# Kernel tuning notes

Hardware: AMD Instinct MI355X
Metric: run time of the kernel (lower is better)

The kernel has to match this reference:

```python
import jax, jax.numpy as jnp
import numpy as np

B, T, K, D = 32, 512, 4, 256
E, M = 100000, 2048
NEG = -10000000000.0


def setup_inputs() -> dict:
    key = jax.random.key(0)
    ks = jax.random.split(key, 8)
    token_reprs = jax.random.normal(ks[0], (B, T, K, D), dtype=jnp.float32)
    edge_index = jax.random.randint(ks[1], (2, E), 0, B * T, dtype=jnp.int64)
    lm_indices = jax.random.randint(ks[2], (M,), 0, B * T * K, dtype=jnp.int64)
    batch_pointers = jax.random.randint(ks[3], (M,), 0, B, dtype=jnp.int64)
    tree_padding_mask = jax.random.bernoulli(ks[4], 0.8, (B, T))
    # SwiGLU(2*dim, 4*dim, 1) parameters (no biases)
    sg = 1.0 / np.sqrt(2 * D)
    sh = 1.0 / np.sqrt(4 * D)
    Wg = jax.random.normal(ks[5], (2 * D, 4 * D), dtype=jnp.float32) * sg
    Wv = jax.random.normal(ks[6], (2 * D, 4 * D), dtype=jnp.float32) * sg
    Wo = jax.random.normal(ks[7], (4 * D, 1), dtype=jnp.float32) * sh
    return {
        "token_reprs": token_reprs,
        "Wg": Wg,
        "Wv": Wv,
        "Wo": Wo,
        "edge_index": edge_index,
        "lm_indices": lm_indices,
        "batch_pointers": batch_pointers,
        "tree_padding_mask": tree_padding_mask,
    }


def reference(token_reprs, Wg, Wv, Wo, edge_index, lm_indices, batch_pointers, tree_padding_mask):
    b, t, k, d = token_reprs.shape
    # predict_lemmas: gather type reprs via edge_index, concat, SwiGLU MLP
    type_flat = token_reprs[:, :, 0].reshape(b * t, d)           # [B*T, D]
    scope_ids, goal_ids = edge_index[0], edge_index[1]
    x = jnp.concatenate([type_flat[scope_ids], type_flat[goal_ids]], axis=-1)  # [E, 2D]
    h = jax.nn.silu(x @ Wg) * (x @ Wv)                           # [E, 4D]
    lemmas = (h @ Wo).squeeze(-1)                                # [E]
    # predict_masks: gathers + masked dot-product scoring
    mask_reprs = token_reprs.reshape(-1, d)[lm_indices]          # [M, D]
    type_reprs = token_reprs[:, :, 0]                            # [B, T, D]
    candidates = type_reprs[batch_pointers]                      # [M, T, D]
    candidate_mask = tree_padding_mask[batch_pointers]           # [M, T]
    lm_preds = jnp.einsum('md,mtd->mt', mask_reprs, candidates)  # [M, T]
    lm_preds = jnp.where(candidate_mask, lm_preds, NEG)
    return lemmas, lm_preds
```

## Files before the change

kernel.cpp:

```cpp
#include <hip/hip_runtime.h>
#include <hip/hip_bf16.h>

typedef __bf16 bf16x8 __attribute__((ext_vector_type(8)));
typedef int   i32x8 __attribute__((ext_vector_type(8)));
typedef float f32x4 __attribute__((ext_vector_type(4)));

#define KDIM 512
#define NDIM 1024
#define DDIM 256
#define TDIM 512
#define MDIM 2048
#define NROWS 16384
#define NEGV -1e10f
#define NLM 128
#define WARR 524288

__device__ __forceinline__ unsigned int pk8(float a, float b, float c, float d) {
    unsigned int p = (unsigned int)__builtin_amdgcn_cvt_pk_fp8_f32(a, b, 0, 0);
    return (unsigned int)__builtin_amdgcn_cvt_pk_fp8_f32(c, d, (int)p, 1);
}

typedef const __attribute__((address_space(1))) unsigned int* gas_p;
typedef __attribute__((address_space(3))) unsigned int* las_p;
__device__ __forceinline__ void gl2lds16(const void* g, void* l) {
    __builtin_amdgcn_global_load_lds((gas_p)g, (las_p)l, 16, 0, 0);
}

__global__ void prep_all(const float* __restrict__ tok,
                         const float* __restrict__ Wg,
                         const float* __restrict__ Wv,
                         const int* __restrict__ bp,
                         unsigned char* __restrict__ tf8,
                         unsigned char* __restrict__ wp8,
                         int* __restrict__ counts,
                         unsigned short* __restrict__ lists) {
    const int bid = blockIdx.x;
    const int tid = threadIdx.x;
    if (bid < 4096) {
        int g = (bid * 256 + tid) * 4;
        int i = g >> 8, c = g & 255;
        float4 v = *(const float4*)(tok + (size_t)i * 1024 + c);
        *(unsigned int*)(tf8 + g) = pk8(v.x, v.y, v.z, v.w);
    } else if (bid < 4608) {
        __shared__ float tg[32][33];
        __shared__ float tv[32][33];
        int pb = bid - 4096;
        int n0 = (pb & 31) * 32, k0 = (pb >> 5) * 32;
        {
            int kk = tid >> 3, nn = (tid & 7) * 4;
            float4 g = *(const float4*)(Wg + (size_t)(k0 + kk) * NDIM + n0 + nn);
            float4 v = *(const float4*)(Wv + (size_t)(k0 + kk) * NDIM + n0 + nn);
            tg[kk][nn] = g.x; tg[kk][nn + 1] = g.y; tg[kk][nn + 2] = g.z; tg[kk][nn + 3] = g.w;
            tv[kk][nn] = v.x; tv[kk][nn + 1] = v.y; tv[kk][nn + 2] = v.z; tv[kk][nn + 3] = v.w;
        }
        __syncthreads();
        int nn2 = tid >> 3, kk2 = (tid & 7) * 4;
        unsigned int pg = pk8(tg[kk2][nn2], tg[kk2 + 1][nn2],
                              tg[kk2 + 2][nn2], tg[kk2 + 3][nn2]);
        unsigned int pv = pk8(tv[kk2][nn2], tv[kk2 + 1][nn2],
                              tv[kk2 + 2][nn2], tv[kk2 + 3][nn2]);
        int n = n0 + nn2, k = k0 + kk2;
        int nt = n >> 6, wn = (n >> 5) & 1, ni = (n >> 4) & 1, cp = n & 15;
        int kc = k >> 7, rem = k & 127, qq = rem >> 5, hh = (rem >> 4) & 1, bb = rem & 15;
        int frag = ((nt * 4 + kc) * 2 + wn) * 2 + ni;
        size_t off = (size_t)frag * 2048 + (qq * 16 + cp) * 32 + hh * 16 + bb;
        *(unsigned int*)(wp8 + off) = pg;
        *(unsigned int*)(wp8 + WARR + off) = pv;
    } else {
        __shared__ int c[32];
        if (tid < 32) c[tid] = 0;
        __syncthreads();
        for (int m = tid; m < MDIM; m += 256) {
            int b = bp[m];
            int pos = atomicAdd(&c[b], 1);
            lists[b * MDIM + pos] = (unsigned short)m;
        }
        __syncthreads();
        if (tid < 32) counts[tid] = c[tid];
    }
}

__launch_bounds__(256, 2)
__global__ void fused_main(const unsigned char* __restrict__ tf8,
                           const unsigned char* __restrict__ wp8,
                           const float* __restrict__ Wo,
                           const int* __restrict__ scope,
                           const int* __restrict__ goal,
                           float* __restrict__ outLem, int E,
                           const float* __restrict__ tok,
                           const int* __restrict__ lmi,
                           const int* __restrict__ counts,
                           const unsigned short* __restrict__ lists,
                           const int* __restrict__ tpm,
                           float* __restrict__ outP) {
    __shared__ unsigned char sA[64 * 1024];
    __shared__ float sRed[256];

    const int tid = threadIdx.x;
    const int lane = tid & 63;
    const int w = tid >> 6;
    const int col = lane & 15;
    const int q = lane >> 4;

    if ((int)blockIdx.x < NLM) {
        const int lb = blockIdx.x;
        const int b = lb & 31;
        const int t0 = (lb >> 5) * 128;
        const int cnt = counts[b];
        for (int mt = w * 16; mt < cnt; mt += 64) {
            int mc = mt + col;
            int aid = lists[b * MDIM + (mc < cnt ? mc : cnt - 1)];
            const float* arow = tok + (size_t)lmi[aid] * DDIM;
            i32x8 af[2];
#pragma unroll
            for (int kc = 0; kc < 2; kc++) {
                unsigned int d[8];
#pragma unroll
                for (int j = 0; j < 8; j++) {
                    float4 v = *(const float4*)(arow + kc * 128 + q * 32 + j * 4);
                    d[j] = pk8(v.x, v.y, v.z, v.w);
                }
                af[kc] = (i32x8){(int)d[0], (int)d[1], (int)d[2], (int)d[3],
                                 (int)d[4], (int)d[5], (int)d[6], (int)d[7]};
            }
            int gm[4];
#pragma unroll
            for (int r = 0; r < 4; r++) {
                int mrow = mt + q * 4 + r;
                gm[r] = (mrow < cnt) ? (int)lists[b * MDIM + mrow] : -1;
            }
#pragma unroll
            for (int ntile = 0; ntile < 8; ntile++) {
                int t = t0 + ntile * 16 + col;
                const unsigned char* brow = tf8 + (size_t)(b * TDIM + t) * DDIM;
                f32x4 acc = (f32x4){0.f, 0.f, 0.f, 0.f};
#pragma unroll
                for (int kc = 0; kc < 2; kc++) {
                    uint4 lo = *(const uint4*)(brow + kc * 128 + q * 32);
                    uint4 hi = *(const uint4*)(brow + kc * 128 + q * 32 + 16);
                    i32x8 bf = (i32x8){(int)lo.x, (int)lo.y, (int)lo.z, (int)lo.w,
                                       (int)hi.x, (int)hi.y, (int)hi.z, (int)hi.w};
                    acc = __builtin_amdgcn_mfma_scale_f32_16x16x128_f8f6f4(
                        af[kc], bf, acc, 0, 0, 0, 0x7F7F7F7F, 0, 0x7F7F7F7F);
                }
                int pmv = tpm[b * TDIM + t];
#pragma unroll
                for (int r = 0; r < 4; r++) {
                    if (gm[r] >= 0)
                        outP[(size_t)gm[r] * TDIM + t] = pmv ? acc[r] : NEGV;
                }
            }
        }
        return;
    }

    const int bx = blockIdx.x - NLM;
    const int etile = bx * 128;
    const int wm = w & 1;
    const int wn = w >> 1;

#pragma unroll
    for (int i = 0; i < 16; i++) {
        int r = w * 16 + i;
        int j = r & 1, kc = (r >> 1) & 3, mi = (r >> 3) & 3, am = r >> 5;
        int row = am * 64 + mi * 16 + col;
        int e = etile + row;
        int id = (e < E) ? ((kc < 2) ? scope[e] : goal[e]) : 0;
        gl2lds16(tf8 + (size_t)id * DDIM + (kc & 1) * 128 + q * 32 + j * 16,
                 &sA[r * 1024]);
    }
    __syncthreads();

    float lem[16];
#pragma unroll
    for (int i = 0; i < 16; i++) lem[i] = 0.f;

    const unsigned char* wbase = wp8 + lane * 32;

#define LOADB(s, buf)                                                          \
    {                                                                          \
        _Pragma("unroll")                                                      \
        for (int ni_ = 0; ni_ < 2; ni_++) {                                    \
            size_t f_ = (size_t)(((s) * 2 + wn) * 2 + ni_) * 2048;             \
            uint4 lo_ = *(const uint4*)(wbase + f_);                           \
            uint4 hi_ = *(const uint4*)(wbase + f_ + 16);                      \
            bgb[buf][ni_] = (i32x8){(int)lo_.x, (int)lo_.y, (int)lo_.z,        \
                (int)lo_.w, (int)hi_.x, (int)hi_.y, (int)hi_.z, (int)hi_.w};   \
            lo_ = *(const uint4*)(wbase + WARR + f_);                          \
            hi_ = *(const uint4*)(wbase + WARR + f_ + 16);                     \
            bvb[buf][ni_] = (i32x8){(int)lo_.x, (int)lo_.y, (int)lo_.z,        \
                (int)lo_.w, (int)hi_.x, (int)hi_.y, (int)hi_.z, (int)hi_.w};   \
        }                                                                      \
    }

    i32x8 bgb[2][2], bvb[2][2];
    LOADB(0, 0)

    for (int nt = 0; nt < 16; nt++) {
        f32x4 accG[4][2], accV[4][2];
#pragma unroll
        for (int mi = 0; mi < 4; mi++)
#pragma unroll
            for (int ni = 0; ni < 2; ni++) {
                accG[mi][ni] = (f32x4){0.f, 0.f, 0.f, 0.f};
                accV[mi][ni] = (f32x4){0.f, 0.f, 0.f, 0.f};
            }
#pragma unroll
        for (int kc = 0; kc < 4; kc++) {
            const int cur = kc & 1, nxt = cur ^ 1;
            LOADB(nt * 4 + kc + 1, nxt)
#pragma unroll
            for (int mi = 0; mi < 4; mi++) {
                int rb = ((wm * 4 + mi) * 4 + kc) * 2;
                uint4 lo = *(const uint4*)(&sA[rb * 1024 + lane * 16]);
                uint4 hi = *(const uint4*)(&sA[(rb + 1) * 1024 + lane * 16]);
                i32x8 af = (i32x8){(int)lo.x, (int)lo.y, (int)lo.z, (int)lo.w,
                                   (int)hi.x, (int)hi.y, (int)hi.z, (int)hi.w};
#pragma unroll
                for (int ni = 0; ni < 2; ni++) {
                    accG[mi][ni] = __builtin_amdgcn_mfma_scale_f32_16x16x128_f8f6f4(
                        af, bgb[cur][ni], accG[mi][ni], 0, 0, 0,
                        0x7F7F7F7F, 0, 0x7F7F7F7F);
                    accV[mi][ni] = __builtin_amdgcn_mfma_scale_f32_16x16x128_f8f6f4(
                        af, bvb[cur][ni], accV[mi][ni], 0, 0, 0,
                        0x7F7F7F7F, 0, 0x7F7F7F7F);
                }
            }
        }
#pragma unroll
        for (int ni = 0; ni < 2; ni++) {
            float wo = Wo[nt * 64 + wn * 32 + ni * 16 + col];
#pragma unroll
            for (int mi = 0; mi < 4; mi++)
#pragma unroll
                for (int r = 0; r < 4; r++) {
                    float g = accG[mi][ni][r];
                    float v = accV[mi][ni][r];
                    float s = g * __builtin_amdgcn_rcpf(1.f + __expf(-g));
                    lem[mi * 4 + r] += s * v * wo;
                }
        }
    }
#pragma unroll
    for (int i = 0; i < 16; i++) {
        float v = lem[i];
        for (int off = 8; off > 0; off >>= 1) v += __shfl_xor(v, off, 16);
        if (col == 0) {
            int row = wm * 64 + (i >> 2) * 16 + q * 4 + (i & 3);
            sRed[wn * 128 + row] = v;
        }
    }
    __syncthreads();
    if (tid < 128) {
        int e = etile + tid;
        if (e < E) outLem[e] = sRed[tid] + sRed[128 + tid];
    }
}

extern "C" void kernel_launch(void* const* d_in, const int* in_sizes, int n_in,
                              void* d_out, int out_size, void* d_ws, size_t ws_size,
                              hipStream_t stream) {
    const float* tok = (const float*)d_in[0];
    const float* Wg  = (const float*)d_in[1];
    const float* Wv  = (const float*)d_in[2];
    const float* Wo  = (const float*)d_in[3];
    const int* edge = (const int*)d_in[4];
    const int* lmi  = (const int*)d_in[5];
    const int* bp   = (const int*)d_in[6];
    const int* tpm  = (const int*)d_in[7];
    const int E = in_sizes[4] / 2;
    float* out = (float*)d_out;

    unsigned char* tf8 = (unsigned char*)d_ws;
    unsigned char* wp8 = tf8 + (size_t)NROWS * DDIM;
    int* counts = (int*)(wp8 + 2 * WARR);
    unsigned short* lists = (unsigned short*)(counts + 32);

    prep_all<<<dim3(4609), dim3(256), 0, stream>>>(
        tok, Wg, Wv, bp, tf8, wp8, counts, lists);
    int nLemBlocks = (E + 127) / 128;
    fused_main<<<dim3(NLM + nLemBlocks), dim3(256), 0, stream>>>(
        tf8, wp8, Wo, edge, edge + E, out, E,
        tok, lmi, counts, lists, tpm, out + E);
}
```

Before: 230.0 us.

## Halve lemma edge tile to 64 rows and split N across four warps

Shrinks the lemma SwiGLU block tile from 128 to 64 edges. The four warps now each own a 16-column slice of the hidden dimension instead of a 2x2 M/N split, and partial dot products are reduced over four warps. This halves the shared-memory A tile and raises launch bounds to four blocks per CU, aiming for more latency hiding. In exchange the grid has twice as many blocks, each streaming the full fp8 Wg/Wv weights, so weight traffic through L2 roughly doubles and A-fragment LDS reads per MFMA increase.

Measured after the change: 548.8 us. +138.6%, slower.

```diff
diff --git a/kernel.cpp b/kernel.cpp
--- a/kernel.cpp
+++ b/kernel.cpp
@@ -80,7 +80,7 @@
     }
 }
 
-__launch_bounds__(256, 2)
+__launch_bounds__(256, 4)
 __global__ void fused_main(const unsigned char* __restrict__ tf8,
                            const unsigned char* __restrict__ wp8,
                            const float* __restrict__ Wo,
@@ -93,7 +93,7 @@
                            const unsigned short* __restrict__ lists,
                            const int* __restrict__ tpm,
                            float* __restrict__ outP) {
-    __shared__ unsigned char sA[64 * 1024];
+    __shared__ unsigned char sA[32 * 1024];
     __shared__ float sRed[256];
 
     const int tid = threadIdx.x;
@@ -155,15 +155,13 @@
     }
 
     const int bx = blockIdx.x - NLM;
-    const int etile = bx * 128;
-    const int wm = w & 1;
-    const int wn = w >> 1;
-
-#pragma unroll
-    for (int i = 0; i < 16; i++) {
-        int r = w * 16 + i;
-        int j = r & 1, kc = (r >> 1) & 3, mi = (r >> 3) & 3, am = r >> 5;
-        int row = am * 64 + mi * 16 + col;
+    const int etile = bx * 64;
+
+#pragma unroll
+    for (int i = 0; i < 8; i++) {
+        int r = w * 8 + i;
+        int j = r & 1, kc = (r >> 1) & 3;
+        int row = (r >> 3) * 16 + col;
         int e = etile + row;
         int id = (e < E) ? ((kc < 2) ? scope[e] : goal[e]) : 0;
         gl2lds16(tf8 + (size_t)id * DDIM + (kc & 1) * 128 + q * 32 + j * 16,
@@ -175,85 +173,75 @@
 #pragma unroll
     for (int i = 0; i < 16; i++) lem[i] = 0.f;
 
-    const unsigned char* wbase = wp8 + lane * 32;
+    const unsigned char* wbase = wp8 + lane * 32 + (size_t)w * 2048;
 
 #define LOADB(s, buf)                                                          \
     {                                                                          \
-        _Pragma("unroll")                                                      \
-        for (int ni_ = 0; ni_ < 2; ni_++) {                                    \
-            size_t f_ = (size_t)(((s) * 2 + wn) * 2 + ni_) * 2048;             \
-            uint4 lo_ = *(const uint4*)(wbase + f_);                           \
-            uint4 hi_ = *(const uint4*)(wbase + f_ + 16);                      \
-            bgb[buf][ni_] = (i32x8){(int)lo_.x, (int)lo_.y, (int)lo_.z,        \
-                (int)lo_.w, (int)hi_.x, (int)hi_.y, (int)hi_.z, (int)hi_.w};   \
-            lo_ = *(const uint4*)(wbase + WARR + f_);                          \
-            hi_ = *(const uint4*)(wbase + WARR + f_ + 16);                     \
-            bvb[buf][ni_] = (i32x8){(int)lo_.x, (int)lo_.y, (int)lo_.z,        \
-                (int)lo_.w, (int)hi_.x, (int)hi_.y, (int)hi_.z, (int)hi_.w};   \
-        }                                                                      \
-    }
-
-    i32x8 bgb[2][2], bvb[2][2];
+        size_t f_ = (size_t)(s) * 8192;                                        \
+        uint4 lo_ = *(const uint4*)(wbase + f_);                               \
+        uint4 hi_ = *(const uint4*)(wbase + f_ + 16);                          \
+        bgb[buf] = (i32x8){(int)lo_.x, (int)lo_.y, (int)lo_.z, (int)lo_.w,     \
+                           (int)hi_.x, (int)hi_.y, (int)hi_.z, (int)hi_.w};    \
+        lo_ = *(const uint4*)(wbase + WARR + f_);                              \
+        hi_ = *(const uint4*)(wbase + WARR + f_ + 16);                         \
+        bvb[buf] = (i32x8){(int)lo_.x, (int)lo_.y, (int)lo_.z, (int)lo_.w,     \
+                           (int)hi_.x, (int)hi_.y, (int)hi_.z, (int)hi_.w};    \
+    }
+
+    i32x8 bgb[2], bvb[2];
     LOADB(0, 0)
 
     for (int nt = 0; nt < 16; nt++) {
-        f32x4 accG[4][2], accV[4][2];
-#pragma unroll
-        for (int mi = 0; mi < 4; mi++)
-#pragma unroll
-            for (int ni = 0; ni < 2; ni++) {
-                accG[mi][ni] = (f32x4){0.f, 0.f, 0.f, 0.f};
-                accV[mi][ni] = (f32x4){0.f, 0.f, 0.f, 0.f};
-            }
+        f32x4 accG[4], accV[4];
+#pragma unroll
+        for (int mi = 0; mi < 4; mi++) {
+            accG[mi] = (f32x4){0.f, 0.f, 0.f, 0.f};
+            accV[mi] = (f32x4){0.f, 0.f, 0.f, 0.f};
+        }
 #pragma unroll
         for (int kc = 0; kc < 4; kc++) {
             const int cur = kc & 1, nxt = cur ^ 1;
             LOADB(nt * 4 + kc + 1, nxt)
 #pragma unroll
             for (int mi = 0; mi < 4; mi++) {
-                int rb = ((wm * 4 + mi) * 4 + kc) * 2;
+                int rb = (mi * 4 + kc) * 2;
                 uint4 lo = *(const uint4*)(&sA[rb * 1024 + lane * 16]);
                 uint4 hi = *(const uint4*)(&sA[(rb + 1) * 1024 + lane * 16]);
                 i32x8 af = (i32x8){(int)lo.x, (int)lo.y, (int)lo.z, (int)lo.w,
                                    (int)hi.x, (int)hi.y, (int)hi.z, (int)hi.w};
-#pragma unroll
-                for (int ni = 0; ni < 2; ni++) {
-                    accG[mi][ni] = __builtin_amdgcn_mfma_scale_f32_16x16x128_f8f6f4(
-                        af, bgb[cur][ni], accG[mi][ni], 0, 0, 0,
-                        0x7F7F7F7F, 0, 0x7F7F7F7F);
-                    accV[mi][ni] = __builtin_amdgcn_mfma_scale_f32_16x16x128_f8f6f4(
-                        af, bvb[cur][ni], accV[mi][ni], 0, 0, 0,
-                        0x7F7F7F7F, 0, 0x7F7F7F7F);
-                }
-            }
-        }
-#pragma unroll
-        for (int ni = 0; ni < 2; ni++) {
-            float wo = Wo[nt * 64 + wn * 32 + ni * 16 + col];
-#pragma unroll
-            for (int mi = 0; mi < 4; mi++)
-#pragma unroll
-                for (int r = 0; r < 4; r++) {
-                    float g = accG[mi][ni][r];
-                    float v = accV[mi][ni][r];
-                    float s = g * __builtin_amdgcn_rcpf(1.f + __expf(-g));
-                    lem[mi * 4 + r] += s * v * wo;
-                }
-        }
+                accG[mi] = __builtin_amdgcn_mfma_scale_f32_16x16x128_f8f6f4(
+                    af, bgb[cur], accG[mi], 0, 0, 0,
+                    0x7F7F7F7F, 0, 0x7F7F7F7F);
+                accV[mi] = __builtin_amdgcn_mfma_scale_f32_16x16x128_f8f6f4(
+                    af, bvb[cur], accV[mi], 0, 0, 0,
+                    0x7F7F7F7F, 0, 0x7F7F7F7F);
+            }
+        }
+        float wo = Wo[nt * 64 + w * 16 + col];
+#pragma unroll
+        for (int mi = 0; mi < 4; mi++)
+#pragma unroll
+            for (int r = 0; r < 4; r++) {
+                float g = accG[mi][r];
+                float v = accV[mi][r];
+                float s = g * __builtin_amdgcn_rcpf(1.f + __expf(-g));
+                lem[mi * 4 + r] += s * v * wo;
+            }
     }
 #pragma unroll
     for (int i = 0; i < 16; i++) {
         float v = lem[i];
         for (int off = 8; off > 0; off >>= 1) v += __shfl_xor(v, off, 16);
         if (col == 0) {
-            int row = wm * 64 + (i >> 2) * 16 + q * 4 + (i & 3);
-            sRed[wn * 128 + row] = v;
+            int row = (i >> 2) * 16 + q * 4 + (i & 3);
+            sRed[w * 64 + row] = v;
         }
     }
     __syncthreads();
-    if (tid < 128) {
+    if (tid < 64) {
         int e = etile + tid;
-        if (e < E) outLem[e] = sRed[tid] + sRed[128 + tid];
+        if (e < E)
+            outLem[e] = sRed[tid] + sRed[64 + tid] + sRed[128 + tid] + sRed[192 + tid];
     }
 }
 
@@ -278,7 +266,7 @@
 
     prep_all<<<dim3(4609), dim3(256), 0, stream>>>(
         tok, Wg, Wv, bp, tf8, wp8, counts, lists);
-    int nLemBlocks = (E + 127) / 128;
+    int nLemBlocks = (E + 63) / 64;
     fused_main<<<dim3(NLM + nLemBlocks), dim3(256), 0, stream>>>(
         tf8, wp8, Wo, edge, edge + E, out, E,
         tok, lmi, counts, lists, tpm, out + E);
```
